# Kernel optimization log

Hardware: AMD Instinct MI355X
Metric: run time of the kernel (lower is better)

## Reference

```python
import jax, jax.numpy as jnp
import numpy as np

N_NODES = 100000


def gcn_conv(x, edge_index, W, b, n):
    # PyG GCNConv: add self-loops, symmetric normalization, then scatter-add.
    src, dst = edge_index[0], edge_index[1]
    loop = jnp.arange(n, dtype=src.dtype)
    src = jnp.concatenate([src, loop])
    dst = jnp.concatenate([dst, loop])
    h = x @ W  # [n, out]
    deg = jnp.zeros((n,), dtype=x.dtype).at[dst].add(1.0)
    dinv = jnp.where(deg > 0, jax.lax.rsqrt(deg), 0.0)
    norm = dinv[src] * dinv[dst]  # [E+n]
    msg = h[src] * norm[:, None]  # gather + scale
    out = jax.ops.segment_sum(msg, dst, num_segments=n)  # scatter-add
    return out + b


def setup_inputs() -> dict:
    key = jax.random.key(0)
    ks = jax.random.split(key, 6)
    n, f, h, c, e = N_NODES, 128, 32, 7, 3200000
    x = jax.random.normal(ks[0], (n, f), dtype=jnp.float32)
    edge_index = jax.random.randint(ks[1], (2, e), 0, n, dtype=jnp.int64)
    W1 = jax.random.normal(ks[2], (f, h), dtype=jnp.float32) * (1.0 / np.sqrt(f))
    b1 = jnp.zeros((h,), dtype=jnp.float32)
    W2 = jax.random.normal(ks[3], (h, c), dtype=jnp.float32) * (1.0 / np.sqrt(h))
    b2 = jnp.zeros((c,), dtype=jnp.float32)
    return {"x": x, "edge_index": edge_index, "W1": W1, "b1": b1, "W2": W2, "b2": b2}


def reference(x, edge_index, W1, b1, W2, b2):
    n = x.shape[0]
    h = jax.nn.relu(gcn_conv(x, edge_index, W1, b1, n))
    # F.dropout(training=False) is identity in eval mode
    out = gcn_conv(h, edge_index, W2, b2, n)
    return jax.nn.log_softmax(out, axis=1)
```

## Files before the change

kernel.cpp:

```cpp
#include <hip/hip_runtime.h>
#include <math.h>


#define F_IN   128
#define F_HID  32
#define F_OUT  7
#define TILE   8192
#define BSH    8
#define BNODES 256
#define HSZ    512
#define PCAP   10240
#define QSH    13
#define NQ     16

typedef __attribute__((ext_vector_type(8))) short bf16x8;
typedef __attribute__((ext_vector_type(4))) float f32x4;
typedef __attribute__((ext_vector_type(4))) int   i32x4;

__device__ __forceinline__ float bf2f(unsigned short u) {
    return __uint_as_float(((unsigned int)u) << 16);
}
__device__ __forceinline__ unsigned short f2bf(float f) {
    unsigned int u = __float_as_uint(f);
    u += 0x7FFF + ((u >> 16) & 1);
    return (unsigned short)(u >> 16);
}
__device__ __forceinline__ unsigned int pack2(unsigned short lo, unsigned short hi) {
    return (unsigned int)lo | ((unsigned int)hi << 16);
}
#define NTL(p) __builtin_nontemporal_load(p)

__device__ __forceinline__ void acc8(float* a, uint4 v) {
    a[0] += bf2f((unsigned short)v.x); a[1] += bf2f((unsigned short)(v.x >> 16));
    a[2] += bf2f((unsigned short)v.y); a[3] += bf2f((unsigned short)(v.y >> 16));
    a[4] += bf2f((unsigned short)v.z); a[5] += bf2f((unsigned short)(v.z >> 16));
    a[6] += bf2f((unsigned short)v.w); a[7] += bf2f((unsigned short)(v.w >> 16));
}

__global__ __launch_bounds__(512)
void k_tileHist(const int* __restrict__ dst, int E, int NB, int* __restrict__ counts,
                const float* __restrict__ W1, unsigned short* __restrict__ Wfrag) {
    __shared__ int h[HSZ];
    int tile = blockIdx.x, t = threadIdx.x;
    if (tile == 0) {
        for (int idx = t; idx < 4096; idx += 512) {
            int j = idx & 7;
            int l = (idx >> 3) & 63;
            int f = idx >> 9;
            int nt = f >> 2, ks = f & 3;
            int k = ks * 32 + ((l >> 4) << 3) + j;
            int col = nt * 16 + (l & 15);
            Wfrag[idx] = f2bf(W1[k * F_HID + col]);
        }
    }
    for (int i = t; i < NB; i += 512) h[i] = 0;
    __syncthreads();
    int base = tile * TILE;
    int lim = base + TILE; if (lim > E) lim = E;
    int n4 = (lim - base) >> 2;
    const i32x4* d4 = (const i32x4*)(dst + base);
    for (int i = t; i < n4; i += 512) {
        i32x4 d = NTL(&d4[i]);
        atomicAdd(&h[d[0] >> BSH], 1);
        atomicAdd(&h[d[1] >> BSH], 1);
        atomicAdd(&h[d[2] >> BSH], 1);
        atomicAdd(&h[d[3] >> BSH], 1);
    }
    __syncthreads();
    for (int i = t; i < NB; i += 512) counts[tile * NB + i] = h[i];
}

__global__ void k_scanA(const int* __restrict__ counts, int NSCAN, int NB, int NT,
                        int* __restrict__ bsum) {
    __shared__ int s[1024];
    int t = threadIdx.x;
    int idx = blockIdx.x * 1024 + t;
    int v = 0;
    if (idx < NSCAN) { int b = idx / NT, tt = idx - b * NT; v = counts[tt * NB + b]; }
    s[t] = v;
    __syncthreads();
    for (int off = 512; off > 0; off >>= 1) {
        if (t < off) s[t] += s[t + off];
        __syncthreads();
    }
    if (t == 0) bsum[blockIdx.x] = s[0];
}

__global__ void k_scanB(int* __restrict__ bsum, int nb) {
    __shared__ int s[1024];
    int t = threadIdx.x;
    int v = (t < nb) ? bsum[t] : 0;
    s[t] = v;
    __syncthreads();
    for (int off = 1; off < 1024; off <<= 1) {
        int a = (t >= off) ? s[t - off] : 0;
        __syncthreads();
        s[t] += a;
        __syncthreads();
    }
    if (t < nb) bsum[t] = s[t] - v;
}

__global__ void k_scanC(const int* __restrict__ counts, int NSCAN, int NB, int NT,
                        const int* __restrict__ bsum, int* __restrict__ tileOffset) {
    __shared__ int s[1024];
    int t = threadIdx.x;
    int idx = blockIdx.x * 1024 + t;
    int v = 0;
    if (idx < NSCAN) { int b = idx / NT, tt = idx - b * NT; v = counts[tt * NB + b]; }
    s[t] = v;
    __syncthreads();
    for (int off = 1; off < 1024; off <<= 1) {
        int a = (t >= off) ? s[t - off] : 0;
        __syncthreads();
        s[t] += a;
        __syncthreads();
    }
    if (idx < NSCAN) tileOffset[idx] = bsum[blockIdx.x] + s[t] - v;
}

__global__ __launch_bounds__(512)
void k_tileFill(const int* __restrict__ src, const int* __restrict__ dst,
                int E, int NB, int NT, const int* __restrict__ tileOffset,
                int* __restrict__ pairBuf) {
    __shared__ int lcur[HSZ];
    int bid = blockIdx.x;
    int xcd = bid & 7;
    int idx = bid >> 3;
    int q = NT >> 3, r = NT & 7;
    int tile = (xcd < r ? xcd * (q + 1) : r * (q + 1) + (xcd - r) * q) + idx;
    int t = threadIdx.x;
    for (int i = t; i < NB; i += 512) lcur[i] = tileOffset[i * NT + tile];
    __syncthreads();
    int base = tile * TILE;
    int lim = base + TILE; if (lim > E) lim = E;
    int n4 = (lim - base) >> 2;
    const i32x4* s4 = (const i32x4*)(src + base);
    const i32x4* d4 = (const i32x4*)(dst + base);
    for (int i = t; i < n4; i += 512) {
        i32x4 s = NTL(&s4[i]);
        i32x4 d = NTL(&d4[i]);
        #pragma unroll
        for (int k = 0; k < 4; ++k) {
            int b = d[k] >> BSH;
            int pos = atomicAdd(&lcur[b], 1);
            pairBuf[pos] = ((d[k] & (BNODES - 1)) << 17) | s[k];
        }
    }
}

__global__ __launch_bounds__(512)
void k_bucketCSR(const int* __restrict__ pairBuf, const int* __restrict__ tileOffset,
                 int NT, int NB, int E, int n,
                 int* __restrict__ degi, int* __restrict__ cursor,
                 float* __restrict__ dinv, int* __restrict__ srcSorted) {
    __shared__ int outb[PCAP];
    __shared__ int cntq[BNODES * NQ];
    __shared__ int pref[BNODES * NQ];
    __shared__ int sred[512];
    int b = blockIdx.x, t = threadIdx.x;
    for (int i = t; i < BNODES * NQ; i += 512) cntq[i] = 0;
    __syncthreads();
    int bs = tileOffset[b * NT];
    int be = (b + 1 < NB) ? tileOffset[(b + 1) * NT] : E;
    int sz = be - bs;
    for (int j = bs + t; j < be; j += 512) {
        int p = pairBuf[j];
        int idx = ((p >> 17) << 4) | ((p >> QSH) & (NQ - 1));
        atomicAdd(&cntq[idx], 1);
    }
    __syncthreads();
    int loc[8];
    int base8 = t << 3;
    int sum = 0;
    #pragma unroll
    for (int k = 0; k < 8; ++k) { loc[k] = cntq[base8 + k]; sum += loc[k]; }
    sred[t] = sum;
    __syncthreads();
    for (int off = 1; off < 512; off <<= 1) {
        int a = (t >= off) ? sred[t - off] : 0;
        __syncthreads();
        sred[t] += a;
        __syncthreads();
    }
    int run = sred[t] - sum;
    #pragma unroll
    for (int k = 0; k < 8; ++k) { pref[base8 + k] = run; run += loc[k]; }
    __syncthreads();
    if (t < BNODES) {
        int node = (b << BSH) + t;
        if (node < n) {
            int dsum = 0;
            #pragma unroll
            for (int k = 0; k < NQ; ++k) dsum += cntq[(t << 4) + k];
            degi[node]   = dsum;
            cursor[node] = bs + pref[t << 4];
            dinv[node]   = rsqrtf((float)dsum + 1.0f);
        }
    }
    __syncthreads();
    for (int j = bs + t; j < be; j += 512) {
        int p = pairBuf[j];
        int idx = ((p >> 17) << 4) | ((p >> QSH) & (NQ - 1));
        int pos = atomicAdd(&pref[idx], 1);
        int s = p & 0x1FFFF;
        if (pos < PCAP) outb[pos] = s;
        else            srcSorted[bs + pos] = s;
    }
    __syncthreads();
    int lim = sz < PCAP ? sz : PCAP;
    for (int idx = t; idx < lim; idx += 512) srcSorted[bs + idx] = outb[idx];
}

__global__ void k_gemm1(const float* __restrict__ x, const unsigned short* __restrict__ Wfrag,
                        const float* __restrict__ dinv, unsigned short* __restrict__ g1b,
                        int n) {
    int wave = threadIdx.x >> 6;
    int lane = threadIdx.x & 63;
    int row0 = (blockIdx.x * 4 + wave) * 16;
    if (row0 >= n) return;
    bf16x8 bfr[2][4];
    #pragma unroll
    for (int nt = 0; nt < 2; ++nt)
        #pragma unroll
        for (int ks = 0; ks < 4; ++ks)
            bfr[nt][ks] = *(const bf16x8*)&Wfrag[(((nt << 2) + ks) * 64 + lane) << 3];
    int arow = row0 + (lane & 15);
    const float* xr = x + (size_t)arow * F_IN + ((lane >> 4) << 3);
    f32x4 acc0 = {0.f, 0.f, 0.f, 0.f};
    f32x4 acc1 = {0.f, 0.f, 0.f, 0.f};
    #pragma unroll
    for (int ks = 0; ks < 4; ++ks) {
        f32x4 lo = NTL((const f32x4*)(xr + ks * 32));
        f32x4 hi = NTL((const f32x4*)(xr + ks * 32 + 4));
        bf16x8 a;
        a[0] = (short)f2bf(lo[0]); a[1] = (short)f2bf(lo[1]);
        a[2] = (short)f2bf(lo[2]); a[3] = (short)f2bf(lo[3]);
        a[4] = (short)f2bf(hi[0]); a[5] = (short)f2bf(hi[1]);
        a[6] = (short)f2bf(hi[2]); a[7] = (short)f2bf(hi[3]);
        acc0 = __builtin_amdgcn_mfma_f32_16x16x32_bf16(a, bfr[0][ks], acc0, 0, 0, 0);
        acc1 = __builtin_amdgcn_mfma_f32_16x16x32_bf16(a, bfr[1][ks], acc1, 0, 0, 0);
    }
    int col = lane & 15;
    #pragma unroll
    for (int rr = 0; rr < 4; ++rr) {
        int orow = row0 + ((lane >> 4) << 2) + rr;
        float di = dinv[orow];
        g1b[(size_t)orow * F_HID + col]      = f2bf(acc0[rr] * di);
        g1b[(size_t)orow * F_HID + col + 16] = f2bf(acc1[rr] * di);
    }
}

__global__ void k_gather1l2(const uint4* __restrict__ g1q, const int* __restrict__ srcSorted,
                            const int* __restrict__ cursor, const int* __restrict__ degi,
                            const float* __restrict__ dinv, const float* __restrict__ b1,
                            const float* __restrict__ W2, uint4* __restrict__ g2q, int n) {
    int t = threadIdx.x;
    int c = t & 7;
    int q = c >> 2;
    int f = c & 3;
    int node = blockIdx.x * 32 + (t >> 3);
    if (node >= n) return;
    int start = cursor[node];
    int end = start + degi[node];
    float a[8], b[8];
    #pragma unroll
    for (int k = 0; k < 8; ++k) { a[k] = 0.f; b[k] = 0.f; }
    if (q == 0) acc8(a, g1q[node * 4 + f]);
    int j = start + q;
    for (; j + 6 < end; j += 8) {
        int s0 = srcSorted[j];
        int s1 = srcSorted[j + 2];
        int s2 = srcSorted[j + 4];
        int s3 = srcSorted[j + 6];
        uint4 v0 = g1q[s0 * 4 + f];
        uint4 v1 = g1q[s1 * 4 + f];
        uint4 v2 = g1q[s2 * 4 + f];
        uint4 v3 = g1q[s3 * 4 + f];
        acc8(a, v0); acc8(b, v1); acc8(a, v2); acc8(b, v3);
    }
    for (; j < end; j += 2) acc8(a, g1q[srcSorted[j] * 4 + f]);
    float af[8];
    #pragma unroll
    for (int k = 0; k < 8; ++k) {
        af[k] = a[k] + b[k];
        af[k] += __shfl_xor(af[k], 4, 64);
    }
    float di = dinv[node];
    float h[8];
    #pragma unroll
    for (int k = 0; k < 8; ++k) {
        float v = di * af[k] + b1[8 * f + k];
        h[k] = v > 0.f ? v : 0.f;
    }
    float p[F_OUT];
    #pragma unroll
    for (int k = 0; k < F_OUT; ++k) {
        float s = 0.f;
        #pragma unroll
        for (int f8 = 0; f8 < 8; ++f8) s += h[f8] * W2[(8 * f + f8) * F_OUT + k];
        p[k] = s;
    }
    #pragma unroll
    for (int m = 1; m < 4; m <<= 1) {
        #pragma unroll
        for (int k = 0; k < F_OUT; ++k) p[k] += __shfl_xor(p[k], m, 64);
    }
    if (c == 0) {
        uint4 qv;
        qv.x = pack2(f2bf(di * p[0]), f2bf(di * p[1]));
        qv.y = pack2(f2bf(di * p[2]), f2bf(di * p[3]));
        qv.z = pack2(f2bf(di * p[4]), f2bf(di * p[5]));
        qv.w = pack2(f2bf(di * p[6]), 0);
        g2q[node] = qv;
    }
}

__global__ void k_gather2final(const uint4* __restrict__ g2q,
                               const int* __restrict__ srcSorted,
                               const int* __restrict__ cursor, const int* __restrict__ degi,
                               const float* __restrict__ dinv, const float* __restrict__ b2,
                               float* __restrict__ out, int n) {
    int node = blockIdx.x * 256 + threadIdx.x;
    if (node >= n) return;
    int start = cursor[node];
    int end = start + degi[node];
    float A[8], B[8];
    #pragma unroll
    for (int f = 0; f < 8; ++f) { A[f] = 0.f; B[f] = 0.f; }
    acc8(A, g2q[node]);
    int j = start;
    while (j < end && (j & 3)) { acc8(B, g2q[srcSorted[j]]); ++j; }
    for (; j + 4 <= end; j += 4) {
        i32x4 sA = *(const i32x4*)&srcSorted[j];
        uint4 r0 = g2q[sA[0]];
        uint4 r1 = g2q[sA[1]];
        uint4 r2 = g2q[sA[2]];
        uint4 r3 = g2q[sA[3]];
        acc8(A, r0); acc8(B, r1); acc8(A, r2); acc8(B, r3);
    }
    for (; j < end; ++j) acc8(A, g2q[srcSorted[j]]);
    float di = dinv[node];
    float v[F_OUT];
    float m = -1e30f;
    #pragma unroll
    for (int k = 0; k < F_OUT; ++k) {
        v[k] = di * (A[k] + B[k]) + b2[k];
        m = fmaxf(m, v[k]);
    }
    float ssum = 0.f;
    #pragma unroll
    for (int k = 0; k < F_OUT; ++k) ssum += __expf(v[k] - m);
    float ls = __logf(ssum) + m;
    #pragma unroll
    for (int k = 0; k < F_OUT; ++k)
        __builtin_nontemporal_store(v[k] - ls, &out[node * F_OUT + k]);
}

extern "C" void kernel_launch(void* const* d_in, const int* in_sizes, int n_in,
                              void* d_out, int out_size, void* d_ws, size_t ws_size,
                              hipStream_t stream) {
    const float* x  = (const float*)d_in[0];
    const int*   ei = (const int*)d_in[1];
    const float* W1 = (const float*)d_in[2];
    const float* b1 = (const float*)d_in[3];
    const float* W2 = (const float*)d_in[4];
    const float* b2 = (const float*)d_in[5];
    float* out = (float*)d_out;

    int n = in_sizes[0] / F_IN;
    int E = in_sizes[1] / 2;
    const int* src = ei;
    const int* dst = ei + E;
    int NB = (n + BNODES - 1) >> BSH;
    int NT = (E + TILE - 1) / TILE;
    int NSCAN = NB * NT;
    int nsb = (NSCAN + 1023) / 1024;

    int*            degi       = (int*)d_ws;
    int*            cursor     = degi + n;
    float*          dinv       = (float*)(cursor + n);
    int*            srcSorted  = (int*)(dinv + n);
    int*            pairBuf    = srcSorted + E;
    unsigned short* g1b        = (unsigned short*)pairBuf;
    unsigned short* g2b        = (unsigned short*)(pairBuf + E);
    int*            counts     = (int*)(g2b + (size_t)n * 8);
    int*            tileOffset = counts + NSCAN;
    int*            bsum       = tileOffset + NSCAN;
    unsigned short* Wfrag      = (unsigned short*)(bsum + ((nsb + 3) & ~3));

    k_tileHist<<<NT, 512, 0, stream>>>(dst, E, NB, counts, W1, Wfrag);
    k_scanA<<<nsb, 1024, 0, stream>>>(counts, NSCAN, NB, NT, bsum);
    k_scanB<<<1, 1024, 0, stream>>>(bsum, nsb);
    k_scanC<<<nsb, 1024, 0, stream>>>(counts, NSCAN, NB, NT, bsum, tileOffset);
    k_tileFill<<<NT, 512, 0, stream>>>(src, dst, E, NB, NT, tileOffset, pairBuf);
    k_bucketCSR<<<NB, 512, 0, stream>>>(pairBuf, tileOffset, NT, NB, E, n,
                                        degi, cursor, dinv, srcSorted);
    k_gemm1<<<(n + 63) / 64, 256, 0, stream>>>(x, Wfrag, dinv, g1b, n);
    k_gather1l2<<<(n + 31) / 32, 256, 0, stream>>>((const uint4*)g1b, srcSorted, cursor, degi,
                                                   dinv, b1, W2, (uint4*)g2b, n);
    k_gather2final<<<(n + 255) / 256, 256, 0, stream>>>((const uint4*)g2b, srcSorted, cursor,
                                                        degi, dinv, b2, out, n);
}
```

Before: 142.1 us.

## Fuse layer-1 GEMM into histogram launch and restructure prefix scan

The layer-1 MFMA GEMM now runs as extra blocks inside the histogram kernel, so it overlaps with edge bucketing instead of waiting for the CSR build. Because dinv is not ready at that point, the source-side normalization moves into the layer-1 gather, which now loads dinv[src] per edge. The three-kernel scan becomes a local-scan plus add pass, removing one launch. g1b gets its own workspace region so it no longer aliases pairBuf. The cost is extra dinv gathers in the hot edge loop and per-wave W1 bf16 conversion from global memory.

```diff
diff --git a/kernel.cpp b/kernel.cpp
--- a/kernel.cpp
+++ b/kernel.cpp
@@ -30,6 +30,12 @@
 }
 #define NTL(p) __builtin_nontemporal_load(p)
 
+__device__ __forceinline__ void acc8s(float* a, uint4 v, float s) {
+    a[0] += s * bf2f((unsigned short)v.x); a[1] += s * bf2f((unsigned short)(v.x >> 16));
+    a[2] += s * bf2f((unsigned short)v.y); a[3] += s * bf2f((unsigned short)(v.y >> 16));
+    a[4] += s * bf2f((unsigned short)v.z); a[5] += s * bf2f((unsigned short)(v.z >> 16));
+    a[6] += s * bf2f((unsigned short)v.w); a[7] += s * bf2f((unsigned short)(v.w >> 16));
+}
 __device__ __forceinline__ void acc8(float* a, uint4 v) {
     a[0] += bf2f((unsigned short)v.x); a[1] += bf2f((unsigned short)(v.x >> 16));
     a[2] += bf2f((unsigned short)v.y); a[3] += bf2f((unsigned short)(v.y >> 16));
@@ -38,40 +44,76 @@
 }
 
 __global__ __launch_bounds__(512)
-void k_tileHist(const int* __restrict__ dst, int E, int NB, int* __restrict__ counts,
-                const float* __restrict__ W1, unsigned short* __restrict__ Wfrag) {
-    __shared__ int h[HSZ];
-    int tile = blockIdx.x, t = threadIdx.x;
-    if (tile == 0) {
-        for (int idx = t; idx < 4096; idx += 512) {
-            int j = idx & 7;
-            int l = (idx >> 3) & 63;
-            int f = idx >> 9;
-            int nt = f >> 2, ks = f & 3;
-            int k = ks * 32 + ((l >> 4) << 3) + j;
-            int col = nt * 16 + (l & 15);
-            Wfrag[idx] = f2bf(W1[k * F_HID + col]);
+void k_histGemm(const int* __restrict__ dst, int E, int NB, int NT,
+                int* __restrict__ counts,
+                const float* __restrict__ x, const float* __restrict__ W1,
+                unsigned short* __restrict__ g1b, int n) {
+    int t = threadIdx.x;
+    if (blockIdx.x < (unsigned)NT) {
+        __shared__ int h[HSZ];
+        int tile = blockIdx.x;
+        for (int i = t; i < NB; i += 512) h[i] = 0;
+        __syncthreads();
+        int base = tile * TILE;
+        int lim = base + TILE; if (lim > E) lim = E;
+        int n4 = (lim - base) >> 2;
+        const i32x4* d4 = (const i32x4*)(dst + base);
+        for (int i = t; i < n4; i += 512) {
+            i32x4 d = NTL(&d4[i]);
+            atomicAdd(&h[d[0] >> BSH], 1);
+            atomicAdd(&h[d[1] >> BSH], 1);
+            atomicAdd(&h[d[2] >> BSH], 1);
+            atomicAdd(&h[d[3] >> BSH], 1);
         }
-    }
-    for (int i = t; i < NB; i += 512) h[i] = 0;
-    __syncthreads();
-    int base = tile * TILE;
-    int lim = base + TILE; if (lim > E) lim = E;
-    int n4 = (lim - base) >> 2;
-    const i32x4* d4 = (const i32x4*)(dst + base);
-    for (int i = t; i < n4; i += 512) {
-        i32x4 d = NTL(&d4[i]);
-        atomicAdd(&h[d[0] >> BSH], 1);
-        atomicAdd(&h[d[1] >> BSH], 1);
-        atomicAdd(&h[d[2] >> BSH], 1);
-        atomicAdd(&h[d[3] >> BSH], 1);
-    }
-    __syncthreads();
-    for (int i = t; i < NB; i += 512) counts[tile * NB + i] = h[i];
-}
-
-__global__ void k_scanA(const int* __restrict__ counts, int NSCAN, int NB, int NT,
-                        int* __restrict__ bsum) {
+        __syncthreads();
+        for (int i = t; i < NB; i += 512) counts[tile * NB + i] = h[i];
+        return;
+    }
+    int gb = blockIdx.x - NT;
+    int wave = t >> 6;
+    int lane = t & 63;
+    int row0 = (gb * 8 + wave) * 16;
+    if (row0 >= n) return;
+    bf16x8 bfr[2][4];
+    #pragma unroll
+    for (int nt = 0; nt < 2; ++nt)
+        #pragma unroll
+        for (int ks = 0; ks < 4; ++ks) {
+            bf16x8 w;
+            #pragma unroll
+            for (int j = 0; j < 8; ++j) {
+                int k = ks * 32 + ((lane >> 4) << 3) + j;
+                w[j] = (short)f2bf(W1[k * F_HID + nt * 16 + (lane & 15)]);
+            }
+            bfr[nt][ks] = w;
+        }
+    int arow = row0 + (lane & 15);
+    const float* xr = x + (size_t)arow * F_IN + ((lane >> 4) << 3);
+    f32x4 acc0 = {0.f, 0.f, 0.f, 0.f};
+    f32x4 acc1 = {0.f, 0.f, 0.f, 0.f};
+    #pragma unroll
+    for (int ks = 0; ks < 4; ++ks) {
+        f32x4 lo = NTL((const f32x4*)(xr + ks * 32));
+        f32x4 hi = NTL((const f32x4*)(xr + ks * 32 + 4));
+        bf16x8 a;
+        a[0] = (short)f2bf(lo[0]); a[1] = (short)f2bf(lo[1]);
+        a[2] = (short)f2bf(lo[2]); a[3] = (short)f2bf(lo[3]);
+        a[4] = (short)f2bf(hi[0]); a[5] = (short)f2bf(hi[1]);
+        a[6] = (short)f2bf(hi[2]); a[7] = (short)f2bf(hi[3]);
+        acc0 = __builtin_amdgcn_mfma_f32_16x16x32_bf16(a, bfr[0][ks], acc0, 0, 0, 0);
+        acc1 = __builtin_amdgcn_mfma_f32_16x16x32_bf16(a, bfr[1][ks], acc1, 0, 0, 0);
+    }
+    int col = lane & 15;
+    #pragma unroll
+    for (int rr = 0; rr < 4; ++rr) {
+        int orow = row0 + ((lane >> 4) << 2) + rr;
+        g1b[(size_t)orow * F_HID + col]      = f2bf(acc0[rr]);
+        g1b[(size_t)orow * F_HID + col + 16] = f2bf(acc1[rr]);
+    }
+}
+
+__global__ void k_scanLocal(const int* __restrict__ counts, int NSCAN, int NB, int NT,
+                            int* __restrict__ tileOffset, int* __restrict__ bsum) {
     __shared__ int s[1024];
     int t = threadIdx.x;
     int idx = blockIdx.x * 1024 + t;
@@ -79,44 +121,30 @@
     if (idx < NSCAN) { int b = idx / NT, tt = idx - b * NT; v = counts[tt * NB + b]; }
     s[t] = v;
     __syncthreads();
+    for (int off = 1; off < 1024; off <<= 1) {
+        int a = (t >= off) ? s[t - off] : 0;
+        __syncthreads();
+        s[t] += a;
+        __syncthreads();
+    }
+    if (idx < NSCAN) tileOffset[idx] = s[t] - v;
+    if (t == 1023) bsum[blockIdx.x] = s[1023];
+}
+
+__global__ void k_scanAdd(int* __restrict__ tileOffset, int NSCAN,
+                          const int* __restrict__ bsum, int nsb) {
+    __shared__ int s[1024];
+    int t = threadIdx.x;
+    int blk = blockIdx.x;
+    s[t] = (t < blk && t < nsb) ? bsum[t] : 0;
+    __syncthreads();
     for (int off = 512; off > 0; off >>= 1) {
         if (t < off) s[t] += s[t + off];
         __syncthreads();
     }
-    if (t == 0) bsum[blockIdx.x] = s[0];
-}
-
-__global__ void k_scanB(int* __restrict__ bsum, int nb) {
-    __shared__ int s[1024];
-    int t = threadIdx.x;
-    int v = (t < nb) ? bsum[t] : 0;
-    s[t] = v;
-    __syncthreads();
-    for (int off = 1; off < 1024; off <<= 1) {
-        int a = (t >= off) ? s[t - off] : 0;
-        __syncthreads();
-        s[t] += a;
-        __syncthreads();
-    }
-    if (t < nb) bsum[t] = s[t] - v;
-}
-
-__global__ void k_scanC(const int* __restrict__ counts, int NSCAN, int NB, int NT,
-                        const int* __restrict__ bsum, int* __restrict__ tileOffset) {
-    __shared__ int s[1024];
-    int t = threadIdx.x;
-    int idx = blockIdx.x * 1024 + t;
-    int v = 0;
-    if (idx < NSCAN) { int b = idx / NT, tt = idx - b * NT; v = counts[tt * NB + b]; }
-    s[t] = v;
-    __syncthreads();
-    for (int off = 1; off < 1024; off <<= 1) {
-        int a = (t >= off) ? s[t - off] : 0;
-        __syncthreads();
-        s[t] += a;
-        __syncthreads();
-    }
-    if (idx < NSCAN) tileOffset[idx] = bsum[blockIdx.x] + s[t] - v;
+    int offv = s[0];
+    int idx = blk * 1024 + t;
+    if (idx < NSCAN) tileOffset[idx] += offv;
 }
 
 __global__ __launch_bounds__(512)
@@ -212,45 +240,6 @@
     for (int idx = t; idx < lim; idx += 512) srcSorted[bs + idx] = outb[idx];
 }
 
-__global__ void k_gemm1(const float* __restrict__ x, const unsigned short* __restrict__ Wfrag,
-                        const float* __restrict__ dinv, unsigned short* __restrict__ g1b,
-                        int n) {
-    int wave = threadIdx.x >> 6;
-    int lane = threadIdx.x & 63;
-    int row0 = (blockIdx.x * 4 + wave) * 16;
-    if (row0 >= n) return;
-    bf16x8 bfr[2][4];
-    #pragma unroll
-    for (int nt = 0; nt < 2; ++nt)
-        #pragma unroll
-        for (int ks = 0; ks < 4; ++ks)
-            bfr[nt][ks] = *(const bf16x8*)&Wfrag[(((nt << 2) + ks) * 64 + lane) << 3];
-    int arow = row0 + (lane & 15);
-    const float* xr = x + (size_t)arow * F_IN + ((lane >> 4) << 3);
-    f32x4 acc0 = {0.f, 0.f, 0.f, 0.f};
-    f32x4 acc1 = {0.f, 0.f, 0.f, 0.f};
-    #pragma unroll
-    for (int ks = 0; ks < 4; ++ks) {
-        f32x4 lo = NTL((const f32x4*)(xr + ks * 32));
-        f32x4 hi = NTL((const f32x4*)(xr + ks * 32 + 4));
-        bf16x8 a;
-        a[0] = (short)f2bf(lo[0]); a[1] = (short)f2bf(lo[1]);
-        a[2] = (short)f2bf(lo[2]); a[3] = (short)f2bf(lo[3]);
-        a[4] = (short)f2bf(hi[0]); a[5] = (short)f2bf(hi[1]);
-        a[6] = (short)f2bf(hi[2]); a[7] = (short)f2bf(hi[3]);
-        acc0 = __builtin_amdgcn_mfma_f32_16x16x32_bf16(a, bfr[0][ks], acc0, 0, 0, 0);
-        acc1 = __builtin_amdgcn_mfma_f32_16x16x32_bf16(a, bfr[1][ks], acc1, 0, 0, 0);
-    }
-    int col = lane & 15;
-    #pragma unroll
-    for (int rr = 0; rr < 4; ++rr) {
-        int orow = row0 + ((lane >> 4) << 2) + rr;
-        float di = dinv[orow];
-        g1b[(size_t)orow * F_HID + col]      = f2bf(acc0[rr] * di);
-        g1b[(size_t)orow * F_HID + col + 16] = f2bf(acc1[rr] * di);
-    }
-}
-
 __global__ void k_gather1l2(const uint4* __restrict__ g1q, const int* __restrict__ srcSorted,
                             const int* __restrict__ cursor, const int* __restrict__ degi,
                             const float* __restrict__ dinv, const float* __restrict__ b1,
@@ -263,10 +252,11 @@
     if (node >= n) return;
     int start = cursor[node];
     int end = start + degi[node];
+    float di = dinv[node];
     float a[8], b[8];
     #pragma unroll
     for (int k = 0; k < 8; ++k) { a[k] = 0.f; b[k] = 0.f; }
-    if (q == 0) acc8(a, g1q[node * 4 + f]);
+    if (q == 0) acc8s(a, g1q[node * 4 + f], di);
     int j = start + q;
     for (; j + 6 < end; j += 8) {
         int s0 = srcSorted[j];
@@ -277,16 +267,16 @@
         uint4 v1 = g1q[s1 * 4 + f];
         uint4 v2 = g1q[s2 * 4 + f];
         uint4 v3 = g1q[s3 * 4 + f];
-        acc8(a, v0); acc8(b, v1); acc8(a, v2); acc8(b, v3);
-    }
-    for (; j < end; j += 2) acc8(a, g1q[srcSorted[j] * 4 + f]);
+        float d0 = dinv[s0], d1 = dinv[s1], d2 = dinv[s2], d3 = dinv[s3];
+        acc8s(a, v0, d0); acc8s(b, v1, d1); acc8s(a, v2, d2); acc8s(b, v3, d3);
+    }
+    for (; j < end; j += 2) { int s0 = srcSorted[j]; acc8s(a, g1q[s0 * 4 + f], dinv[s0]); }
     float af[8];
     #pragma unroll
     for (int k = 0; k < 8; ++k) {
         af[k] = a[k] + b[k];
         af[k] += __shfl_xor(af[k], 4, 64);
     }
-    float di = dinv[node];
     float h[8];
     #pragma unroll
     for (int k = 0; k < 8; ++k) {
@@ -376,27 +366,25 @@
     int NT = (E + TILE - 1) / TILE;
     int NSCAN = NB * NT;
     int nsb = (NSCAN + 1023) / 1024;
+    int ngem = (n + 127) / 128;
 
     int*            degi       = (int*)d_ws;
     int*            cursor     = degi + n;
     float*          dinv       = (float*)(cursor + n);
     int*            srcSorted  = (int*)(dinv + n);
     int*            pairBuf    = srcSorted + E;
-    unsigned short* g1b        = (unsigned short*)pairBuf;
-    unsigned short* g2b        = (unsigned short*)(pairBuf + E);
+    unsigned short* g1b        = (unsigned short*)(pairBuf + E);
+    unsigned short* g2b        = g1b + (size_t)n * F_HID;
     int*            counts     = (int*)(g2b + (size_t)n * 8);
     int*            tileOffset = counts + NSCAN;
     int*            bsum       = tileOffset + NSCAN;
-    unsigned short* Wfrag      = (unsigned short*)(bsum + ((nsb + 3) & ~3));
-
-    k_tileHist<<<NT, 512, 0, stream>>>(dst, E, NB, counts, W1, Wfrag);
-    k_scanA<<<nsb, 1024, 0, stream>>>(counts, NSCAN, NB, NT, bsum);
-    k_scanB<<<1, 1024, 0, stream>>>(bsum, nsb);
-    k_scanC<<<nsb, 1024, 0, stream>>>(counts, NSCAN, NB, NT, bsum, tileOffset);
+
+    k_histGemm<<<NT + ngem, 512, 0, stream>>>(dst, E, NB, NT, counts, x, W1, g1b, n);
+    k_scanLocal<<<nsb, 1024, 0, stream>>>(counts, NSCAN, NB, NT, tileOffset, bsum);
+    k_scanAdd<<<nsb, 1024, 0, stream>>>(tileOffset, NSCAN, bsum, nsb);
     k_tileFill<<<NT, 512, 0, stream>>>(src, dst, E, NB, NT, tileOffset, pairBuf);
     k_bucketCSR<<<NB, 512, 0, stream>>>(pairBuf, tileOffset, NT, NB, E, n,
                                         degi, cursor, dinv, srcSorted);
-    k_gemm1<<<(n + 63) / 64, 256, 0, stream>>>(x, Wfrag, dinv, g1b, n);
     k_gather1l2<<<(n + 31) / 32, 256, 0, stream>>>((const uint4*)g1b, srcSorted, cursor, degi,
                                                    dinv, b1, W2, (uint4*)g2b, n);
     k_gather2final<<<(n + 255) / 256, 256, 0, stream>>>((const uint4*)g2b, srcSorted, cursor,
```

New measurement: 150.2 us. 5.7% more time.
